# Optimization experiments

Measured on AMD Instinct MI355X. Metric: run time of the kernel, lower is better.

The kernel has to match this reference:

```python
import jax, jax.numpy as jnp
import numpy as np

D_MODEL = 1024
NUM_HEADS = 16
D_K = D_MODEL // NUM_HEADS


def setup_inputs() -> dict:
    key = jax.random.key(0)
    ks = jax.random.split(key, 5)
    B, S = 4, 2048
    scale = 1.0 / np.sqrt(D_MODEL)
    x = jax.random.normal(ks[0], (B, S, D_MODEL), dtype=jnp.float32)
    Wq = jax.random.normal(ks[1], (D_MODEL, D_MODEL), dtype=jnp.float32) * scale
    Wk = jax.random.normal(ks[2], (D_MODEL, D_MODEL), dtype=jnp.float32) * scale
    Wv = jax.random.normal(ks[3], (D_MODEL, D_MODEL), dtype=jnp.float32) * scale
    Wo = jax.random.normal(ks[4], (D_MODEL, D_MODEL), dtype=jnp.float32) * scale
    return {"x": x, "Wq": Wq, "Wk": Wk, "Wv": Wv, "Wo": Wo}


def reference(x, Wq, Wk, Wv, Wo):
    B, S, _ = x.shape
    # projections (torch Linear: y = x @ W^T, no bias)
    def proj(W):
        y = jnp.einsum('bsd,ed->bse', x, W)
        # split heads: (b, s, h*dk) -> (b, h, s, dk)
        return y.reshape(B, S, NUM_HEADS, D_K).transpose(0, 2, 1, 3)
    Q, K, V = proj(Wq), proj(Wk), proj(Wv)
    scores = jnp.einsum('bhqd,bhkd->bhqk', Q, K) / np.sqrt(D_K)
    causal = jnp.tril(jnp.ones((S, S), dtype=bool))
    scores = jnp.where(causal, scores, -jnp.inf)
    attn = jax.nn.softmax(scores, axis=-1)
    out = jnp.einsum('bhqk,bhkd->bhqd', attn, V)
    out = out.transpose(0, 2, 1, 3).reshape(B, S, D_MODEL)
    return jnp.einsum('bse,de->bsd', out, Wo)
```

## Files before the change

### kernel.cpp

```cpp
#include <hip/hip_runtime.h>
#include <hip/hip_bf16.h>

typedef __attribute__((ext_vector_type(8))) short short8;
typedef __attribute__((ext_vector_type(2))) float f32x2;
typedef __attribute__((ext_vector_type(4))) float f32x4;
typedef __attribute__((ext_vector_type(16))) float f32x16;

static constexpr int DM = 1024;
static constexpr int NH = 16;
static constexpr int DK = 64;
static constexpr int SL = 2048;
static constexpr int BB = 4;
static constexpr size_t QKV_ELEMS = (size_t)BB * NH * SL * DK;
static constexpr float NEG_BIG = -30000.0f;
static constexpr float SC_LOG2E = 0.125f * 1.44269504088896340736f;

union PackB { __hip_bfloat16 h[8]; uint4 u; };
union Pack4 { __hip_bfloat16 h[4]; uint2 u; };

typedef __attribute__((address_space(1))) unsigned int gu32;
typedef __attribute__((address_space(3))) unsigned int lu32;
__device__ __forceinline__ void async_copy16(const void* g, void* l) {
    __builtin_amdgcn_global_load_lds((gu32*)g, (lu32*)l, 16, 0, 0);
}

__device__ __forceinline__ unsigned cvt_pk_bf16(float lo, float hi) {
    unsigned r;
    asm("v_cvt_pk_bf16_f32 %0, %1, %2" : "=v"(r) : "v"(lo), "v"(hi));
    return r;
}
__device__ __forceinline__ void pl32_swap(unsigned &a, unsigned &b) {
    asm("v_permlane32_swap_b32 %0, %1" : "+v"(a), "+v"(b));
}

__global__ __launch_bounds__(256)
void cvt_all(const float* __restrict__ x,
             const float* __restrict__ wq, const float* __restrict__ wk,
             const float* __restrict__ wv, const float* __restrict__ wo,
             __hip_bfloat16* __restrict__ dst)
{
    const size_t i = (size_t)blockIdx.x * 256 + threadIdx.x;
    const float* src; size_t local;
    if (i < 2097152) { src = x; local = i; }
    else {
        const size_t j = i - 2097152;
        const int r = (int)(j >> 18);
        local = j & 262143;
        src = (r == 0) ? wq : (r == 1) ? wk : (r == 2) ? wv : wo;
    }
    float4 f = reinterpret_cast<const float4*>(src)[local];
    Pack4 p;
    p.h[0] = __float2bfloat16(f.x); p.h[1] = __float2bfloat16(f.y);
    p.h[2] = __float2bfloat16(f.z); p.h[3] = __float2bfloat16(f.w);
    reinterpret_cast<uint2*>(dst)[i] = p.u;
}

__global__ __launch_bounds__(256)
void gemm_qkv(const __hip_bfloat16* __restrict__ A,
              const __hip_bfloat16* __restrict__ W,
              __hip_bfloat16* __restrict__ q_out,
              __hip_bfloat16* __restrict__ k_out,
              __hip_bfloat16* __restrict__ v_out)
{
    __shared__ __hip_bfloat16 As[128 * 64];
    __shared__ __hip_bfloat16 Bs[128 * 64];
    const int tid  = threadIdx.x;
    const int m0   = blockIdx.x * 128;
    const int n0   = blockIdx.y * 128;
    const int w    = tid >> 6;
    const int lane = tid & 63;
    const int quad = lane >> 4;
    const int ln   = lane & 15;
    const int wm   = (w & 1) * 64;
    const int wn   = (w >> 1) * 64;
    const int srow = lane >> 3;
    const int sch  = ((lane & 7) ^ srow) * 8;

    f32x4 acc[4][4] = {};

    for (int k0 = 0; k0 < DM; k0 += 64) {
        #pragma unroll
        for (int j = 0; j < 4; j++) {
            const int rbase = w * 32 + j * 8;
            async_copy16(A + (size_t)(m0 + rbase + srow) * DM + k0 + sch,
                         &As[rbase * 64]);
            async_copy16(W + (size_t)(n0 + rbase + srow) * DM + k0 + sch,
                         &Bs[rbase * 64]);
        }
        __syncthreads();

        #pragma unroll
        for (int ks = 0; ks < 2; ks++) {
            short8 a[4], b[4];
            #pragma unroll
            for (int i = 0; i < 4; i++)
                a[i] = *reinterpret_cast<const short8*>(
                    &As[(wm + i*16 + ln) * 64 + (((ks*4 + quad) ^ (ln & 7)) * 8)]);
            #pragma unroll
            for (int j = 0; j < 4; j++)
                b[j] = *reinterpret_cast<const short8*>(
                    &Bs[(wn + j*16 + ln) * 64 + (((ks*4 + quad) ^ (ln & 7)) * 8)]);
            #pragma unroll
            for (int i = 0; i < 4; i++)
                #pragma unroll
                for (int j = 0; j < 4; j++)
                    acc[i][j] = __builtin_amdgcn_mfma_f32_16x16x32_bf16(a[i], b[j], acc[i][j], 0, 0, 0);
        }
        __syncthreads();
    }

    #pragma unroll
    for (int i = 0; i < 4; i++) {
        #pragma unroll
        for (int j = 0; j < 4; j++) {
            #pragma unroll
            for (int r = 0; r < 4; r++) {
                const int m = m0 + wm + i*16 + quad*4 + r;
                const int n = n0 + wn + j*16 + ln;
                const int b_ = m >> 11;
                const int s  = m & 2047;
                const int which = n >> 10;
                const int nn = n & 1023;
                const int h  = nn >> 6;
                const int d  = nn & 63;
                if (which == 0) {
                    const __hip_bfloat16 v = __float2bfloat16(acc[i][j][r] * SC_LOG2E);
                    q_out[((size_t)((b_*NH + h)*SL + s))*DK + d] = v;
                } else if (which == 1) {
                    const __hip_bfloat16 v = __float2bfloat16(acc[i][j][r]);
                    k_out[((size_t)((b_*NH + h)*SL + s))*DK + d] = v;
                } else {
                    const __hip_bfloat16 v = __float2bfloat16(acc[i][j][r]);
                    v_out[((size_t)((b_*NH + h)*DK + d))*SL + s] = v;
                }
            }
        }
    }
}

__global__ __launch_bounds__(256)
void gemm_wo(const __hip_bfloat16* __restrict__ A,
             const __hip_bfloat16* __restrict__ W,
             float* __restrict__ outp)
{
    __shared__ __hip_bfloat16 As[128 * 64];
    __shared__ __hip_bfloat16 Bs[128 * 64];
    const int tid  = threadIdx.x;
    const int m0   = blockIdx.x * 128;
    const int n0   = blockIdx.y * 128;
    const int w    = tid >> 6;
    const int lane = tid & 63;
    const int quad = lane >> 4;
    const int ln   = lane & 15;
    const int wm   = (w & 1) * 64;
    const int wn   = (w >> 1) * 64;
    const int srow = lane >> 3;
    const int sch  = ((lane & 7) ^ srow) * 8;

    f32x4 acc[4][4] = {};

    for (int k0 = 0; k0 < DM; k0 += 64) {
        #pragma unroll
        for (int j = 0; j < 4; j++) {
            const int rbase = w * 32 + j * 8;
            async_copy16(A + (size_t)(m0 + rbase + srow) * DM + k0 + sch,
                         &As[rbase * 64]);
            async_copy16(W + (size_t)(n0 + rbase + srow) * DM + k0 + sch,
                         &Bs[rbase * 64]);
        }
        __syncthreads();

        #pragma unroll
        for (int ks = 0; ks < 2; ks++) {
            short8 a[4], b[4];
            #pragma unroll
            for (int i = 0; i < 4; i++)
                a[i] = *reinterpret_cast<const short8*>(
                    &As[(wm + i*16 + ln) * 64 + (((ks*4 + quad) ^ (ln & 7)) * 8)]);
            #pragma unroll
            for (int j = 0; j < 4; j++)
                b[j] = *reinterpret_cast<const short8*>(
                    &Bs[(wn + j*16 + ln) * 64 + (((ks*4 + quad) ^ (ln & 7)) * 8)]);
            #pragma unroll
            for (int i = 0; i < 4; i++)
                #pragma unroll
                for (int j = 0; j < 4; j++)
                    acc[i][j] = __builtin_amdgcn_mfma_f32_16x16x32_bf16(a[i], b[j], acc[i][j], 0, 0, 0);
        }
        __syncthreads();
    }

    #pragma unroll
    for (int i = 0; i < 4; i++)
        #pragma unroll
        for (int j = 0; j < 4; j++)
            #pragma unroll
            for (int r = 0; r < 4; r++) {
                const int m = m0 + wm + i*16 + quad*4 + r;
                const int n = n0 + wn + j*16 + ln;
                outp[(size_t)m * DM + n] = acc[i][j][r];
            }
}

template<bool A_BF16, int MODE>
__global__ __launch_bounds__(256)
void gemm_bt(const void* __restrict__ Ap,
             const float* __restrict__ W,
             void* __restrict__ outp, float scl)
{
    __shared__ __hip_bfloat16 As[128][40];
    __shared__ __hip_bfloat16 Bs[128][40];
    const int tid  = threadIdx.x;
    const int m0   = blockIdx.x * 128;
    const int n0   = blockIdx.y * 128;
    const int w    = tid >> 6;
    const int lane = tid & 63;
    const int quad = lane >> 4;
    const int ln   = lane & 15;
    const int wm   = (w & 1) * 64;
    const int wn   = (w >> 1) * 64;
    const int lr   = tid >> 1;
    const int lc   = (tid & 1) * 16;

    f32x4 acc[4][4] = {};

    for (int k0 = 0; k0 < DM; k0 += 32) {
        if (A_BF16) {
            const uint4* ap = reinterpret_cast<const uint4*>(
                (const __hip_bfloat16*)Ap + (size_t)(m0 + lr) * DM + k0 + lc);
            uint4 a0 = ap[0], a1 = ap[1];
            *reinterpret_cast<uint4*>(&As[lr][lc])     = a0;
            *reinterpret_cast<uint4*>(&As[lr][lc + 8]) = a1;
        } else {
            const float4* ap = reinterpret_cast<const float4*>(
                (const float*)Ap + (size_t)(m0 + lr) * DM + k0 + lc);
            float4 f0 = ap[0], f1 = ap[1], f2 = ap[2], f3 = ap[3];
            PackB p0, p1;
            p0.h[0] = __float2bfloat16(f0.x); p0.h[1] = __float2bfloat16(f0.y);
            p0.h[2] = __float2bfloat16(f0.z); p0.h[3] = __float2bfloat16(f0.w);
            p0.h[4] = __float2bfloat16(f1.x); p0.h[5] = __float2bfloat16(f1.y);
            p0.h[6] = __float2bfloat16(f1.z); p0.h[7] = __float2bfloat16(f1.w);
            p1.h[0] = __float2bfloat16(f2.x); p1.h[1] = __float2bfloat16(f2.y);
            p1.h[2] = __float2bfloat16(f2.z); p1.h[3] = __float2bfloat16(f2.w);
            p1.h[4] = __float2bfloat16(f3.x); p1.h[5] = __float2bfloat16(f3.y);
            p1.h[6] = __float2bfloat16(f3.z); p1.h[7] = __float2bfloat16(f3.w);
            *reinterpret_cast<uint4*>(&As[lr][lc])     = p0.u;
            *reinterpret_cast<uint4*>(&As[lr][lc + 8]) = p1.u;
        }
        {
            const float4* wp = reinterpret_cast<const float4*>(
                W + (size_t)(n0 + lr) * DM + k0 + lc);
            float4 f0 = wp[0], f1 = wp[1], f2 = wp[2], f3 = wp[3];
            PackB p0, p1;
            p0.h[0] = __float2bfloat16(f0.x); p0.h[1] = __float2bfloat16(f0.y);
            p0.h[2] = __float2bfloat16(f0.z); p0.h[3] = __float2bfloat16(f0.w);
            p0.h[4] = __float2bfloat16(f1.x); p0.h[5] = __float2bfloat16(f1.y);
            p0.h[6] = __float2bfloat16(f1.z); p0.h[7] = __float2bfloat16(f1.w);
            p1.h[0] = __float2bfloat16(f2.x); p1.h[1] = __float2bfloat16(f2.y);
            p1.h[2] = __float2bfloat16(f2.z); p1.h[3] = __float2bfloat16(f2.w);
            p1.h[4] = __float2bfloat16(f3.x); p1.h[5] = __float2bfloat16(f3.y);
            p1.h[6] = __float2bfloat16(f3.z); p1.h[7] = __float2bfloat16(f3.w);
            *reinterpret_cast<uint4*>(&Bs[lr][lc])     = p0.u;
            *reinterpret_cast<uint4*>(&Bs[lr][lc + 8]) = p1.u;
        }
        __syncthreads();

        short8 a[4], b[4];
        #pragma unroll
        for (int i = 0; i < 4; i++)
            a[i] = *reinterpret_cast<const short8*>(&As[wm + i*16 + ln][quad*8]);
        #pragma unroll
        for (int j = 0; j < 4; j++)
            b[j] = *reinterpret_cast<const short8*>(&Bs[wn + j*16 + ln][quad*8]);
        #pragma unroll
        for (int i = 0; i < 4; i++)
            #pragma unroll
            for (int j = 0; j < 4; j++)
                acc[i][j] = __builtin_amdgcn_mfma_f32_16x16x32_bf16(a[i], b[j], acc[i][j], 0, 0, 0);
        __syncthreads();
    }

    #pragma unroll
    for (int i = 0; i < 4; i++) {
        #pragma unroll
        for (int j = 0; j < 4; j++) {
            #pragma unroll
            for (int r = 0; r < 4; r++) {
                const int m = m0 + wm + i*16 + quad*4 + r;
                const int n = n0 + wn + j*16 + ln;
                const float v = acc[i][j][r] * scl;
                if (MODE == 2) {
                    ((float*)outp)[(size_t)m * DM + n] = v;
                } else {
                    const int b_ = m >> 11;
                    const int s  = m & 2047;
                    const int h  = n >> 6;
                    const int d  = n & 63;
                    size_t idx;
                    if (MODE == 0) idx = ((size_t)((b_*NH + h)*SL + s))*DK + d;
                    else           idx = ((size_t)((b_*NH + h)*DK + d))*SL + s;
                    ((__hip_bfloat16*)outp)[idx] = __float2bfloat16(v);
                }
            }
        }
    }
}

__global__ __launch_bounds__(256)
void attn_causal(const __hip_bfloat16* __restrict__ Q,
                 const __hip_bfloat16* __restrict__ K,
                 const __hip_bfloat16* __restrict__ Vt,
                 __hip_bfloat16* __restrict__ O)
{
    __shared__ __hip_bfloat16 Ks[128][72];
    __shared__ __hip_bfloat16 Vs[64][136];

    const int tid  = threadIdx.x;
    const int w    = tid >> 6;
    const int lane = tid & 63;
    const int ln32 = lane & 31;
    const int hi   = lane >> 5;
    const int bh   = blockIdx.y;
    const int b_   = bh >> 4;
    const int h    = bh & 15;

    const int sr = tid >> 3;
    const int sc = (tid & 7) * 8;

    const __hip_bfloat16* Qb = Q  + (size_t)bh * SL * DK;
    const __hip_bfloat16* Kb = K  + (size_t)bh * SL * DK;
    const __hip_bfloat16* Vb = Vt + (size_t)bh * DK * SL;

    for (int pass = 0; pass < 2; ++pass) {
        const int qt    = (pass == 0) ? (int)blockIdx.x : 15 - (int)blockIdx.x;
        const int q0    = qt * 128;
        const int qbase = q0 + w * 32;
        const int qg    = qbase + ln32;

        short8 qf[4];
        #pragma unroll
        for (int dt = 0; dt < 4; dt++)
            qf[dt] = *reinterpret_cast<const short8*>(
                Qb + (size_t)qg * DK + dt*16 + hi*8);

        f32x16 o0 = {}, o1 = {};
        f32x2 ls2 = {0.f, 0.f};

        const int npair = qt + 1;

        uint4 ka = *reinterpret_cast<const uint4*>(Kb + (size_t)(sr     ) * DK + sc);
        uint4 kb = *reinterpret_cast<const uint4*>(Kb + (size_t)(sr + 32) * DK + sc);
        uint4 kc = *reinterpret_cast<const uint4*>(Kb + (size_t)(sr + 64) * DK + sc);
        uint4 kd = *reinterpret_cast<const uint4*>(Kb + (size_t)(sr + 96) * DK + sc);
        uint4 va = *reinterpret_cast<const uint4*>(Vb + (size_t)(sr     ) * SL + sc);
        uint4 vb = *reinterpret_cast<const uint4*>(Vb + (size_t)(sr + 32) * SL + sc);
        uint4 vc = *reinterpret_cast<const uint4*>(Vb + (size_t)(sr     ) * SL + 64 + sc);
        uint4 vd = *reinterpret_cast<const uint4*>(Vb + (size_t)(sr + 32) * SL + 64 + sc);

        for (int ip = 0; ip < npair; ++ip) {
            const int k0 = ip * 128;
            __syncthreads();
            *reinterpret_cast<uint4*>(&Ks[sr      ][sc]) = ka;
            *reinterpret_cast<uint4*>(&Ks[sr +  32][sc]) = kb;
            *reinterpret_cast<uint4*>(&Ks[sr +  64][sc]) = kc;
            *reinterpret_cast<uint4*>(&Ks[sr +  96][sc]) = kd;
            *reinterpret_cast<uint4*>(&Vs[sr      ][sc]) = va;
            *reinterpret_cast<uint4*>(&Vs[sr +  32][sc]) = vb;
            *reinterpret_cast<uint4*>(&Vs[sr      ][64 + sc]) = vc;
            *reinterpret_cast<uint4*>(&Vs[sr +  32][64 + sc]) = vd;
            __syncthreads();
            if (ip + 1 < npair) {
                const int kn = k0 + 128;
                ka = *reinterpret_cast<const uint4*>(Kb + (size_t)(kn + sr     ) * DK + sc);
                kb = *reinterpret_cast<const uint4*>(Kb + (size_t)(kn + sr + 32) * DK + sc);
                kc = *reinterpret_cast<const uint4*>(Kb + (size_t)(kn + sr + 64) * DK + sc);
                kd = *reinterpret_cast<const uint4*>(Kb + (size_t)(kn + sr + 96) * DK + sc);
                va = *reinterpret_cast<const uint4*>(Vb + (size_t)(sr     ) * SL + kn + sc);
                vb = *reinterpret_cast<const uint4*>(Vb + (size_t)(sr + 32) * SL + kn + sc);
                vc = *reinterpret_cast<const uint4*>(Vb + (size_t)(sr     ) * SL + kn + 64 + sc);
                vd = *reinterpret_cast<const uint4*>(Vb + (size_t)(sr + 32) * SL + kn + 64 + sc);
            }

            #pragma unroll
            for (int hf = 0; hf < 2; hf++) {
                const int kh0 = k0 + hf * 64;
                if (kh0 > qbase + 31) continue;

                f32x16 s0 = {}, s1 = {};
                __builtin_amdgcn_s_setprio(1);
                #pragma unroll
                for (int dt = 0; dt < 4; dt++) {
                    short8 kf0 = *reinterpret_cast<const short8*>(&Ks[hf*64 +      ln32][dt*16 + hi*8]);
                    short8 kf1 = *reinterpret_cast<const short8*>(&Ks[hf*64 + 32 + ln32][dt*16 + hi*8]);
                    s0 = __builtin_amdgcn_mfma_f32_32x32x16_bf16(kf0, qf[dt], s0, 0, 0, 0);
                    s1 = __builtin_amdgcn_mfma_f32_32x32x16_bf16(kf1, qf[dt], s1, 0, 0, 0);
                }
                __builtin_amdgcn_s_setprio(0);

                const bool dodiag = (kh0 + 63 > qbase);
                if (dodiag) {
                    #pragma unroll
                    for (int r = 0; r < 16; r++) {
                        const int km = (r & 3) + 8*(r >> 2) + 4*hi;
                        float v0 = s0[r];
                        float v1 = s1[r];
                        if (kh0 + km      > qg) v0 = NEG_BIG;
                        if (kh0 + 32 + km > qg) v1 = NEG_BIG;
                        const float p0 = __builtin_amdgcn_exp2f(v0);
                        const float p1 = __builtin_amdgcn_exp2f(v1);
                        s0[r] = p0; s1[r] = p1;
                        ls2.x += p0; ls2.y += p1;
                    }
                } else {
                    #pragma unroll
                    for (int r = 0; r < 16; r++) {
                        const float p0 = __builtin_amdgcn_exp2f(s0[r]);
                        const float p1 = __builtin_amdgcn_exp2f(s1[r]);
                        s0[r] = p0; s1[r] = p1;
                        ls2.x += p0; ls2.y += p1;
                    }
                }

                __builtin_amdgcn_s_setprio(1);
                #pragma unroll
                for (int c = 0; c < 4; c++) {
                    const int R = 8 * (c & 1);
                    unsigned x0, x1, y0, y1;
                    if (c < 2) {
                        x0 = cvt_pk_bf16(s0[R+0], s0[R+1]);
                        x1 = cvt_pk_bf16(s0[R+2], s0[R+3]);
                        y0 = cvt_pk_bf16(s0[R+4], s0[R+5]);
                        y1 = cvt_pk_bf16(s0[R+6], s0[R+7]);
                    } else {
                        x0 = cvt_pk_bf16(s1[R+0], s1[R+1]);
                        x1 = cvt_pk_bf16(s1[R+2], s1[R+3]);
                        y0 = cvt_pk_bf16(s1[R+4], s1[R+5]);
                        y1 = cvt_pk_bf16(s1[R+6], s1[R+7]);
                    }
                    pl32_swap(x0, y0);
                    pl32_swap(x1, y1);
                    union { unsigned u[4]; short8 s8; } pf;
                    pf.u[0] = x0; pf.u[1] = x1; pf.u[2] = y0; pf.u[3] = y1;
                    short8 vf0 = *reinterpret_cast<const short8*>(&Vs[ln32     ][hf*64 + c*16 + hi*8]);
                    short8 vf1 = *reinterpret_cast<const short8*>(&Vs[32 + ln32][hf*64 + c*16 + hi*8]);
                    o0 = __builtin_amdgcn_mfma_f32_32x32x16_bf16(vf0, pf.s8, o0, 0, 0, 0);
                    o1 = __builtin_amdgcn_mfma_f32_32x32x16_bf16(vf1, pf.s8, o1, 0, 0, 0);
                }
                __builtin_amdgcn_s_setprio(0);
            }
        }

        float lsum = ls2.x + ls2.y;
        const float ls = lsum + __shfl_xor(lsum, 32, 64);
        const float rq = 1.0f / ls;

        __hip_bfloat16* Orow = O + (((size_t)b_ * SL + qg) * NH + h) * DK;
        #pragma unroll
        for (int g = 0; g < 4; g++) {
            uint2 pk0, pk1;
            pk0.x = cvt_pk_bf16(o0[4*g+0]*rq, o0[4*g+1]*rq);
            pk0.y = cvt_pk_bf16(o0[4*g+2]*rq, o0[4*g+3]*rq);
            pk1.x = cvt_pk_bf16(o1[4*g+0]*rq, o1[4*g+1]*rq);
            pk1.y = cvt_pk_bf16(o1[4*g+2]*rq, o1[4*g+3]*rq);
            *reinterpret_cast<uint2*>(Orow + 8*g + 4*hi)      = pk0;
            *reinterpret_cast<uint2*>(Orow + 32 + 8*g + 4*hi) = pk1;
        }
    }
}

extern "C" void kernel_launch(void* const* d_in, const int* in_sizes, int n_in,
                              void* d_out, int out_size, void* d_ws, size_t ws_size,
                              hipStream_t stream)
{
    const float* x  = (const float*)d_in[0];
    const float* Wq = (const float*)d_in[1];
    const float* Wk = (const float*)d_in[2];
    const float* Wv = (const float*)d_in[3];
    const float* Wo = (const float*)d_in[4];

    __hip_bfloat16* q_ws = (__hip_bfloat16*)d_ws;
    __hip_bfloat16* k_ws = q_ws + QKV_ELEMS;
    __hip_bfloat16* v_ws = k_ws + QKV_ELEMS;

    const dim3 gb(256);
    const size_t FAST_WS = (3 * QKV_ELEMS + QKV_ELEMS + 4 * (size_t)DM * DM)
                           * sizeof(__hip_bfloat16);

    if (ws_size >= FAST_WS) {
        __hip_bfloat16* xb  = v_ws + QKV_ELEMS;
        __hip_bfloat16* wqb = xb  + QKV_ELEMS;
        __hip_bfloat16* wob = wqb + 3 * (size_t)DM * DM;

        cvt_all<<<12288, 256, 0, stream>>>(x, Wq, Wk, Wv, Wo, xb);

        gemm_qkv<<<dim3(64, 24), gb, 0, stream>>>(xb, wqb, q_ws, k_ws, v_ws);

        attn_causal<<<dim3(8, BB*NH), 256, 0, stream>>>(q_ws, k_ws, v_ws, xb);

        gemm_wo<<<dim3(64, 8), gb, 0, stream>>>(xb, wob, (float*)d_out);
    } else {
        __hip_bfloat16* obuf = (__hip_bfloat16*)d_out;
        float*          fbuf = (float*)d_ws;
        const dim3 gg(64, 8);
        gemm_bt<false, 0><<<gg, gb, 0, stream>>>(x, Wq, q_ws, SC_LOG2E);
        gemm_bt<false, 0><<<gg, gb, 0, stream>>>(x, Wk, k_ws, 1.0f);
        gemm_bt<false, 1><<<gg, gb, 0, stream>>>(x, Wv, v_ws, 1.0f);
        attn_causal<<<dim3(8, BB*NH), 256, 0, stream>>>(q_ws, k_ws, v_ws, obuf);
        gemm_bt<true, 2><<<gg, gb, 0, stream>>>(obuf, Wo, fbuf, 1.0f);
        (void)hipMemcpyAsync(d_out, fbuf, QKV_ELEMS * sizeof(float),
                             hipMemcpyDeviceToDevice, stream);
    }
}
```

Measured before the change: 255.7 us.

## Double-buffer GEMM LDS tiles and use async swizzled K/V loads in attention

Both projection GEMMs now use two LDS buffers, prefetching the next K-tile with async global-to-LDS copies while MFMAs run on the current one. This removes one barrier per iteration, and MFMA sections get raised wave priority. The attention kernel replaces register-staged K/V prefetch with direct async LDS copies into XOR-swizzled unpadded tiles. The attention change drops the register prefetch overlap, so each K/V tile load is now waited on before compute. The GEMMs double their LDS use, which may lower occupancy.

Measured after the change: 249.9 us. 1.02x faster.

```diff
diff --git a/kernel.cpp b/kernel.cpp
--- a/kernel.cpp
+++ b/kernel.cpp
@@ -62,8 +62,8 @@
               __hip_bfloat16* __restrict__ k_out,
               __hip_bfloat16* __restrict__ v_out)
 {
-    __shared__ __hip_bfloat16 As[128 * 64];
-    __shared__ __hip_bfloat16 Bs[128 * 64];
+    __shared__ __hip_bfloat16 As[2][128 * 64];
+    __shared__ __hip_bfloat16 Bs[2][128 * 64];
     const int tid  = threadIdx.x;
     const int m0   = blockIdx.x * 128;
     const int n0   = blockIdx.y * 128;
@@ -78,16 +78,25 @@
 
     f32x4 acc[4][4] = {};
 
-    for (int k0 = 0; k0 < DM; k0 += 64) {
+    auto stage = [&](int buf, int k0) {
         #pragma unroll
         for (int j = 0; j < 4; j++) {
             const int rbase = w * 32 + j * 8;
             async_copy16(A + (size_t)(m0 + rbase + srow) * DM + k0 + sch,
-                         &As[rbase * 64]);
+                         &As[buf][rbase * 64]);
             async_copy16(W + (size_t)(n0 + rbase + srow) * DM + k0 + sch,
-                         &Bs[rbase * 64]);
-        }
-        __syncthreads();
+                         &Bs[buf][rbase * 64]);
+        }
+    };
+
+    constexpr int NT = DM / 64;
+    stage(0, 0);
+    asm volatile("s_waitcnt vmcnt(0)" ::: "memory");
+    __syncthreads();
+
+    int cur = 0;
+    for (int t = 0; t < NT; ++t) {
+        if (t + 1 < NT) stage(cur ^ 1, (t + 1) * 64);
 
         #pragma unroll
         for (int ks = 0; ks < 2; ks++) {
@@ -95,18 +104,25 @@
             #pragma unroll
             for (int i = 0; i < 4; i++)
                 a[i] = *reinterpret_cast<const short8*>(
-                    &As[(wm + i*16 + ln) * 64 + (((ks*4 + quad) ^ (ln & 7)) * 8)]);
+                    &As[cur][(wm + i*16 + ln) * 64 + (((ks*4 + quad) ^ (ln & 7)) * 8)]);
             #pragma unroll
             for (int j = 0; j < 4; j++)
                 b[j] = *reinterpret_cast<const short8*>(
-                    &Bs[(wn + j*16 + ln) * 64 + (((ks*4 + quad) ^ (ln & 7)) * 8)]);
+                    &Bs[cur][(wn + j*16 + ln) * 64 + (((ks*4 + quad) ^ (ln & 7)) * 8)]);
+            __builtin_amdgcn_s_setprio(1);
             #pragma unroll
             for (int i = 0; i < 4; i++)
                 #pragma unroll
                 for (int j = 0; j < 4; j++)
                     acc[i][j] = __builtin_amdgcn_mfma_f32_16x16x32_bf16(a[i], b[j], acc[i][j], 0, 0, 0);
-        }
-        __syncthreads();
+            __builtin_amdgcn_s_setprio(0);
+        }
+
+        if (t + 1 < NT) {
+            asm volatile("s_waitcnt vmcnt(0)" ::: "memory");
+            __syncthreads();
+        }
+        cur ^= 1;
     }
 
     #pragma unroll
@@ -143,8 +159,8 @@
              const __hip_bfloat16* __restrict__ W,
              float* __restrict__ outp)
 {
-    __shared__ __hip_bfloat16 As[128 * 64];
-    __shared__ __hip_bfloat16 Bs[128 * 64];
+    __shared__ __hip_bfloat16 As[2][128 * 64];
+    __shared__ __hip_bfloat16 Bs[2][128 * 64];
     const int tid  = threadIdx.x;
     const int m0   = blockIdx.x * 128;
     const int n0   = blockIdx.y * 128;
@@ -159,16 +175,25 @@
 
     f32x4 acc[4][4] = {};
 
-    for (int k0 = 0; k0 < DM; k0 += 64) {
+    auto stage = [&](int buf, int k0) {
         #pragma unroll
         for (int j = 0; j < 4; j++) {
             const int rbase = w * 32 + j * 8;
             async_copy16(A + (size_t)(m0 + rbase + srow) * DM + k0 + sch,
-                         &As[rbase * 64]);
+                         &As[buf][rbase * 64]);
             async_copy16(W + (size_t)(n0 + rbase + srow) * DM + k0 + sch,
-                         &Bs[rbase * 64]);
-        }
-        __syncthreads();
+                         &Bs[buf][rbase * 64]);
+        }
+    };
+
+    constexpr int NT = DM / 64;
+    stage(0, 0);
+    asm volatile("s_waitcnt vmcnt(0)" ::: "memory");
+    __syncthreads();
+
+    int cur = 0;
+    for (int t = 0; t < NT; ++t) {
+        if (t + 1 < NT) stage(cur ^ 1, (t + 1) * 64);
 
         #pragma unroll
         for (int ks = 0; ks < 2; ks++) {
@@ -176,18 +201,25 @@
             #pragma unroll
             for (int i = 0; i < 4; i++)
                 a[i] = *reinterpret_cast<const short8*>(
-                    &As[(wm + i*16 + ln) * 64 + (((ks*4 + quad) ^ (ln & 7)) * 8)]);
+                    &As[cur][(wm + i*16 + ln) * 64 + (((ks*4 + quad) ^ (ln & 7)) * 8)]);
             #pragma unroll
             for (int j = 0; j < 4; j++)
                 b[j] = *reinterpret_cast<const short8*>(
-                    &Bs[(wn + j*16 + ln) * 64 + (((ks*4 + quad) ^ (ln & 7)) * 8)]);
+                    &Bs[cur][(wn + j*16 + ln) * 64 + (((ks*4 + quad) ^ (ln & 7)) * 8)]);
+            __builtin_amdgcn_s_setprio(1);
             #pragma unroll
             for (int i = 0; i < 4; i++)
                 #pragma unroll
                 for (int j = 0; j < 4; j++)
                     acc[i][j] = __builtin_amdgcn_mfma_f32_16x16x32_bf16(a[i], b[j], acc[i][j], 0, 0, 0);
-        }
-        __syncthreads();
+            __builtin_amdgcn_s_setprio(0);
+        }
+
+        if (t + 1 < NT) {
+            asm volatile("s_waitcnt vmcnt(0)" ::: "memory");
+            __syncthreads();
+        }
+        cur ^= 1;
     }
 
     #pragma unroll
@@ -312,8 +344,8 @@
                  const __hip_bfloat16* __restrict__ Vt,
                  __hip_bfloat16* __restrict__ O)
 {
-    __shared__ __hip_bfloat16 Ks[128][72];
-    __shared__ __hip_bfloat16 Vs[64][136];
+    __shared__ __hip_bfloat16 Ks[128 * 64];
+    __shared__ __hip_bfloat16 Vs[64 * 128];
 
     const int tid  = threadIdx.x;
     const int w    = tid >> 6;
@@ -324,9 +356,6 @@
     const int b_   = bh >> 4;
     const int h    = bh & 15;
 
-    const int sr = tid >> 3;
-    const int sc = (tid & 7) * 8;
-
     const __hip_bfloat16* Qb = Q  + (size_t)bh * SL * DK;
     const __hip_bfloat16* Kb = K  + (size_t)bh * SL * DK;
     const __hip_bfloat16* Vb = Vt + (size_t)bh * DK * SL;
@@ -348,38 +377,24 @@
 
         const int npair = qt + 1;
 
-        uint4 ka = *reinterpret_cast<const uint4*>(Kb + (size_t)(sr     ) * DK + sc);
-        uint4 kb = *reinterpret_cast<const uint4*>(Kb + (size_t)(sr + 32) * DK + sc);
-        uint4 kc = *reinterpret_cast<const uint4*>(Kb + (size_t)(sr + 64) * DK + sc);
-        uint4 kd = *reinterpret_cast<const uint4*>(Kb + (size_t)(sr + 96) * DK + sc);
-        uint4 va = *reinterpret_cast<const uint4*>(Vb + (size_t)(sr     ) * SL + sc);
-        uint4 vb = *reinterpret_cast<const uint4*>(Vb + (size_t)(sr + 32) * SL + sc);
-        uint4 vc = *reinterpret_cast<const uint4*>(Vb + (size_t)(sr     ) * SL + 64 + sc);
-        uint4 vd = *reinterpret_cast<const uint4*>(Vb + (size_t)(sr + 32) * SL + 64 + sc);
-
         for (int ip = 0; ip < npair; ++ip) {
             const int k0 = ip * 128;
+            #pragma unroll
+            for (int j = 0; j < 4; j++) {
+                const int rb = w * 32 + j * 8;
+                const int r  = rb + (lane >> 3);
+                async_copy16(Kb + (size_t)(k0 + r) * DK + (((lane & 7) ^ (r & 7)) * 8),
+                             &Ks[rb * 64]);
+            }
+            #pragma unroll
+            for (int j = 0; j < 4; j++) {
+                const int db = w * 16 + j * 4;
+                const int d  = db + (lane >> 4);
+                async_copy16(Vb + (size_t)d * SL + k0 + (((lane & 15) ^ (d & 7)) * 8),
+                             &Vs[db * 128]);
+            }
+            asm volatile("s_waitcnt vmcnt(0)" ::: "memory");
             __syncthreads();
-            *reinterpret_cast<uint4*>(&Ks[sr      ][sc]) = ka;
-            *reinterpret_cast<uint4*>(&Ks[sr +  32][sc]) = kb;
-            *reinterpret_cast<uint4*>(&Ks[sr +  64][sc]) = kc;
-            *reinterpret_cast<uint4*>(&Ks[sr +  96][sc]) = kd;
-            *reinterpret_cast<uint4*>(&Vs[sr      ][sc]) = va;
-            *reinterpret_cast<uint4*>(&Vs[sr +  32][sc]) = vb;
-            *reinterpret_cast<uint4*>(&Vs[sr      ][64 + sc]) = vc;
-            *reinterpret_cast<uint4*>(&Vs[sr +  32][64 + sc]) = vd;
-            __syncthreads();
-            if (ip + 1 < npair) {
-                const int kn = k0 + 128;
-                ka = *reinterpret_cast<const uint4*>(Kb + (size_t)(kn + sr     ) * DK + sc);
-                kb = *reinterpret_cast<const uint4*>(Kb + (size_t)(kn + sr + 32) * DK + sc);
-                kc = *reinterpret_cast<const uint4*>(Kb + (size_t)(kn + sr + 64) * DK + sc);
-                kd = *reinterpret_cast<const uint4*>(Kb + (size_t)(kn + sr + 96) * DK + sc);
-                va = *reinterpret_cast<const uint4*>(Vb + (size_t)(sr     ) * SL + kn + sc);
-                vb = *reinterpret_cast<const uint4*>(Vb + (size_t)(sr + 32) * SL + kn + sc);
-                vc = *reinterpret_cast<const uint4*>(Vb + (size_t)(sr     ) * SL + kn + 64 + sc);
-                vd = *reinterpret_cast<const uint4*>(Vb + (size_t)(sr + 32) * SL + kn + 64 + sc);
-            }
 
             #pragma unroll
             for (int hf = 0; hf < 2; hf++) {
@@ -390,8 +405,10 @@
                 __builtin_amdgcn_s_setprio(1);
                 #pragma unroll
                 for (int dt = 0; dt < 4; dt++) {
-                    short8 kf0 = *reinterpret_cast<const short8*>(&Ks[hf*64 +      ln32][dt*16 + hi*8]);
-                    short8 kf1 = *reinterpret_cast<const short8*>(&Ks[hf*64 + 32 + ln32][dt*16 + hi*8]);
+                    const int r0 = hf*64 + ln32;
+                    const int ch = (dt*2 + hi) ^ (ln32 & 7);
+                    short8 kf0 = *reinterpret_cast<const short8*>(&Ks[r0*64 + ch*8]);
+                    short8 kf1 = *reinterpret_cast<const short8*>(&Ks[(r0 + 32)*64 + ch*8]);
                     s0 = __builtin_amdgcn_mfma_f32_32x32x16_bf16(kf0, qf[dt], s0, 0, 0, 0);
                     s1 = __builtin_amdgcn_mfma_f32_32x32x16_bf16(kf1, qf[dt], s1, 0, 0, 0);
                 }
@@ -441,13 +458,15 @@
                     pl32_swap(x1, y1);
                     union { unsigned u[4]; short8 s8; } pf;
                     pf.u[0] = x0; pf.u[1] = x1; pf.u[2] = y0; pf.u[3] = y1;
-                    short8 vf0 = *reinterpret_cast<const short8*>(&Vs[ln32     ][hf*64 + c*16 + hi*8]);
-                    short8 vf1 = *reinterpret_cast<const short8*>(&Vs[32 + ln32][hf*64 + c*16 + hi*8]);
+                    const int vc = (hf*8 + c*2 + hi) ^ (ln32 & 7);
+                    short8 vf0 = *reinterpret_cast<const short8*>(&Vs[ln32*128 + vc*8]);
+                    short8 vf1 = *reinterpret_cast<const short8*>(&Vs[(32 + ln32)*128 + vc*8]);
                     o0 = __builtin_amdgcn_mfma_f32_32x32x16_bf16(vf0, pf.s8, o0, 0, 0, 0);
                     o1 = __builtin_amdgcn_mfma_f32_32x32x16_bf16(vf1, pf.s8, o1, 0, 0, 0);
                 }
                 __builtin_amdgcn_s_setprio(0);
             }
+            __syncthreads();
         }
 
         float lsum = ls2.x + ls2.y;
```
